# Optimization experiments

Hardware: AMD Instinct MI355X
Metric: run time of the kernel (lower is better)

The kernel has to match this reference:

```python
import jax, jax.numpy as jnp
import numpy as np

OUT, IN, BLK = 11008, 4096, 128

def setup_inputs() -> dict:
    key = jax.random.key(0)
    k1, k2, k3, k4, k5 = jax.random.split(key, 5)
    x = jax.random.normal(k1, (64, IN), dtype=jnp.float32)
    weight = jax.random.randint(k2, (OUT, IN // 2), 0, 256, dtype=jnp.int32)  # packed uint4 pairs
    scale = jax.random.uniform(k3, (OUT, 1, BLK), dtype=jnp.float32) * 0.01 + 1e-4
    zp = jax.random.randint(k4, (OUT, 1, BLK), 0, 16).astype(jnp.float32)
    bias = jax.random.normal(k5, (OUT,), dtype=jnp.float32)
    return {"x": x, "weight": weight, "scale": scale, "zp": zp, "bias": bias}

def reference(x, weight, scale, zp, bias):
    dtype = x.dtype
    # unpack: high nibble first, then low nibble (interleaved along in_features)
    w_h = (weight >> 4) & 15
    w_l = weight & 15
    w_unpacked = jnp.stack((w_h, w_l), axis=-1).reshape(OUT, IN)
    # block-wise dequant: scale/zp shaped [OUT, 1, BLK], broadcast over block index dim
    w_blocked = w_unpacked.reshape(OUT, IN // BLK, BLK).astype(dtype)
    w_rec = ((w_blocked - zp.astype(dtype)) * scale.astype(dtype)).reshape(OUT, IN)
    return x @ w_rec.T + bias
```

## Files before the change

### kernel.cpp

```cpp
#include <hip/hip_runtime.h>

#define OUT_F 11008
#define IN_F  4096
#define PKW   2048
#define BLKQ  128
#define MROWS 64

typedef __attribute__((ext_vector_type(8))) short          s16x8;
typedef __attribute__((ext_vector_type(8))) unsigned short u16x8;
typedef __attribute__((ext_vector_type(4))) float          f32x4;
typedef __attribute__((ext_vector_type(4))) int            i32x4;

__device__ __forceinline__ unsigned short f2bf(float f) {
    union { float f; unsigned u; } v; v.f = f;
    unsigned r = v.u + 0x8000u + ((v.u >> 16) & 1u);
    return (unsigned short)(r >> 16);
}

__global__ void prep_xfrag(const float* __restrict__ x, unsigned short* __restrict__ xf) {
    int kb   = blockIdx.x;
    int t    = threadIdx.x;
    int mt   = t >> 6;
    int lane = t & 63;
    int m  = mt * 16 + (lane & 15);
    int k0 = kb * 32 + (lane >> 4) * 8;
    const float* xp = x + m * IN_F + k0;
    f32x4 a = *(const f32x4*)(xp);
    f32x4 b = *(const f32x4*)(xp + 4);
    u16x8 v;
    v[0] = f2bf(a[0]); v[1] = f2bf(a[1]); v[2] = f2bf(a[2]); v[3] = f2bf(a[3]);
    v[4] = f2bf(b[0]); v[5] = f2bf(b[1]); v[6] = f2bf(b[2]); v[7] = f2bf(b[3]);
    *(u16x8*)(xf + (size_t)((kb * 4 + mt) * 64 + lane) * 8) = v;
}

__global__ __launch_bounds__(256) void qlin_main(
    const int*   __restrict__ wq,
    const float* __restrict__ scale,
    const float* __restrict__ zp,
    const float* __restrict__ bias,
    const unsigned short* __restrict__ xf,
    float* __restrict__ out)
{
    __shared__ __align__(16) unsigned short smem[4 * 16 * 136];

    const int t      = threadIdx.x;
    const int o_base = blockIdx.x * 16;
    const int wave   = t >> 6;
    const int lane   = t & 63;

    const int d      = t & 3;
    const int row_r  = (t >> 2) & 15;
    const int region = t >> 6;

    float s[32], zs[32];
    {
        const float* sp = scale + (size_t)(o_base + row_r) * BLKQ + d * 32;
        const float* zpp = zp   + (size_t)(o_base + row_r) * BLKQ + d * 32;
        #pragma unroll
        for (int i = 0; i < 8; ++i) {
            f32x4 sv = *(const f32x4*)(sp  + i * 4);
            f32x4 zv = *(const f32x4*)(zpp + i * 4);
            #pragma unroll
            for (int c = 0; c < 4; ++c) {
                s [i * 4 + c] = sv[c];
                zs[i * 4 + c] = zv[c] * sv[c];
            }
        }
    }

    const int* wbase = wq + (size_t)(o_base + row_r) * PKW + region * 512 + d * 16;
    unsigned short* myw = smem + (region * 16 + row_r) * 136 + d * 32;

    f32x4 acc[4];
    #pragma unroll
    for (int mt = 0; mt < 4; ++mt) acc[mt] = (f32x4){0.f, 0.f, 0.f, 0.f};

    i32x4 wreg[4];
    #pragma unroll
    for (int q = 0; q < 4; ++q) wreg[q] = *(const i32x4*)(wbase + q * 4);

    const s16x8* xfv = (const s16x8*)xf;
    const unsigned short* bbase = smem + (wave * 16 + (lane & 15)) * 136;
    const int quad = lane >> 4;

    for (int tt = 0; tt < 8; ++tt) {
        __syncthreads();

        #pragma unroll
        for (int q = 0; q < 4; ++q) {
            u16x8 ob;
            #pragma unroll
            for (int pp = 0; pp < 4; ++pp) {
                unsigned dw = (unsigned)wreg[q][pp];
                int p = q * 4 + pp;
                float fh = (float)((dw >> 4) & 15u);
                float fl = (float)(dw & 15u);
                ob[2 * pp]     = f2bf(fmaf(fh, s[2 * p],     -zs[2 * p]));
                ob[2 * pp + 1] = f2bf(fmaf(fl, s[2 * p + 1], -zs[2 * p + 1]));
            }
            *(u16x8*)(myw + q * 8) = ob;
        }

        if (tt < 7) {
            const int* nb = wbase + (tt + 1) * 64;
            #pragma unroll
            for (int q = 0; q < 4; ++q) wreg[q] = *(const i32x4*)(nb + q * 4);
        }

        __syncthreads();

        #pragma unroll
        for (int q0 = 0; q0 < 4; ++q0) {
            s16x8 bfrag = *(const s16x8*)(bbase + q0 * 32 + quad * 8);
            int kb = wave * 32 + tt * 4 + q0;
            #pragma unroll
            for (int mt = 0; mt < 4; ++mt) {
                s16x8 afrag = xfv[(size_t)(kb * 4 + mt) * 64 + lane];
                acc[mt] = __builtin_amdgcn_mfma_f32_16x16x32_bf16(afrag, bfrag, acc[mt], 0, 0, 0);
            }
        }
    }

    __syncthreads();
    float* lf = (float*)smem;
    {
        const int col = lane & 15;
        #pragma unroll
        for (int mt = 0; mt < 4; ++mt) {
            #pragma unroll
            for (int r = 0; r < 4; ++r) {
                int m = mt * 16 + quad * 4 + r;
                lf[wave * 1024 + m * 16 + col] = acc[mt][r];
            }
        }
    }
    __syncthreads();
    #pragma unroll
    for (int p = 0; p < 4; ++p) {
        int e = p * 256 + t;
        int m = e >> 4, col = e & 15;
        float v = lf[e] + lf[1024 + e] + lf[2048 + e] + lf[3072 + e] + bias[o_base + col];
        out[(size_t)m * OUT_F + o_base + col] = v;
    }
}

extern "C" void kernel_launch(void* const* d_in, const int* in_sizes, int n_in,
                              void* d_out, int out_size, void* d_ws, size_t ws_size,
                              hipStream_t stream) {
    const float* x     = (const float*)d_in[0];
    const int*   wq    = (const int*)d_in[1];
    const float* scale = (const float*)d_in[2];
    const float* zpv   = (const float*)d_in[3];
    const float* bias  = (const float*)d_in[4];
    float* out = (float*)d_out;
    unsigned short* xf = (unsigned short*)d_ws;

    prep_xfrag<<<128, 256, 0, stream>>>(x, xf);
    qlin_main<<<OUT_F / 16, 256, 0, stream>>>(wq, scale, zpv, bias, xf, out);
}
```

Before: 159.8 us.

## Dequantize weights directly into MFMA B fragments and double-buffer loads

Each lane now loads the packed weights and scale/zero-point values that match its own MFMA B-fragment position and dequantizes them in registers. This removes the LDS staging buffer and the two barriers per iteration. The activation fragments and the next weight group are prefetched into double-buffered registers so global loads overlap the MFMA work. The cost is more register pressure and smaller, strided weight loads per lane (16-byte reads at a 64-byte stride), which may coalesce less well than before.

```diff
diff --git a/kernel.cpp b/kernel.cpp
--- a/kernel.cpp
+++ b/kernel.cpp
@@ -4,7 +4,6 @@
 #define IN_F  4096
 #define PKW   2048
 #define BLKQ  128
-#define MROWS 64
 
 typedef __attribute__((ext_vector_type(8))) short          s16x8;
 typedef __attribute__((ext_vector_type(8))) unsigned short u16x8;
@@ -41,97 +40,89 @@
     const unsigned short* __restrict__ xf,
     float* __restrict__ out)
 {
-    __shared__ __align__(16) unsigned short smem[4 * 16 * 136];
+    __shared__ float lsum[4 * 1024];
 
     const int t      = threadIdx.x;
     const int o_base = blockIdx.x * 16;
     const int wave   = t >> 6;
     const int lane   = t & 63;
+    const int o_r    = lane & 15;
+    const int quad   = lane >> 4;
+    const int o      = o_base + o_r;
 
-    const int d      = t & 3;
-    const int row_r  = (t >> 2) & 15;
-    const int region = t >> 6;
-
-    float s[32], zs[32];
+    float s[4][8], zs[4][8];
     {
-        const float* sp = scale + (size_t)(o_base + row_r) * BLKQ + d * 32;
-        const float* zpp = zp   + (size_t)(o_base + row_r) * BLKQ + d * 32;
+        const float* sp  = scale + (size_t)o * BLKQ + quad * 8;
+        const float* zpp = zp    + (size_t)o * BLKQ + quad * 8;
         #pragma unroll
-        for (int i = 0; i < 8; ++i) {
-            f32x4 sv = *(const f32x4*)(sp  + i * 4);
-            f32x4 zv = *(const f32x4*)(zpp + i * 4);
+        for (int c4 = 0; c4 < 4; ++c4) {
+            f32x4 s0 = *(const f32x4*)(sp  + c4 * 32);
+            f32x4 s1 = *(const f32x4*)(sp  + c4 * 32 + 4);
+            f32x4 z0 = *(const f32x4*)(zpp + c4 * 32);
+            f32x4 z1 = *(const f32x4*)(zpp + c4 * 32 + 4);
             #pragma unroll
-            for (int c = 0; c < 4; ++c) {
-                s [i * 4 + c] = sv[c];
-                zs[i * 4 + c] = zv[c] * sv[c];
+            for (int i = 0; i < 4; ++i) {
+                s [c4][i]     = s0[i];  zs[c4][i]     = z0[i] * s0[i];
+                s [c4][i + 4] = s1[i];  zs[c4][i + 4] = z1[i] * s1[i];
             }
         }
     }
 
-    const int* wbase = wq + (size_t)(o_base + row_r) * PKW + region * 512 + d * 16;
-    unsigned short* myw = smem + (region * 16 + row_r) * 136 + d * 32;
+    const int* wb = wq + (size_t)o * PKW + wave * 512 + quad * 4;
+    const s16x8* xfv = (const s16x8*)xf;
+    const int kb0 = wave * 32;
 
     f32x4 acc[4];
     #pragma unroll
     for (int mt = 0; mt < 4; ++mt) acc[mt] = (f32x4){0.f, 0.f, 0.f, 0.f};
 
-    i32x4 wreg[4];
+    i32x4 wgrp[2][4];
+    s16x8 af[2][4];
+
     #pragma unroll
-    for (int q = 0; q < 4; ++q) wreg[q] = *(const i32x4*)(wbase + q * 4);
+    for (int cc = 0; cc < 4; ++cc) wgrp[0][cc] = *(const i32x4*)(wb + cc * 16);
+    #pragma unroll
+    for (int mt = 0; mt < 4; ++mt) af[0][mt] = xfv[(size_t)((kb0 * 4 + mt) * 64) + lane];
 
-    const s16x8* xfv = (const s16x8*)xf;
-    const unsigned short* bbase = smem + (wave * 16 + (lane & 15)) * 136;
-    const int quad = lane >> 4;
-
-    for (int tt = 0; tt < 8; ++tt) {
-        __syncthreads();
-
+    #pragma unroll
+    for (int g = 0; g < 8; ++g) {
+        const int pg = g & 1;
+        if (g < 7) {
+            const int* nb = wb + (g + 1) * 64;
+            #pragma unroll
+            for (int cc = 0; cc < 4; ++cc) wgrp[pg ^ 1][cc] = *(const i32x4*)(nb + cc * 16);
+        }
         #pragma unroll
-        for (int q = 0; q < 4; ++q) {
-            u16x8 ob;
+        for (int cc = 0; cc < 4; ++cc) {
+            const int kk = g * 4 + cc;
+            const int pb = kk & 1;
+            if (kk < 31) {
+                const int kbn = kb0 + kk + 1;
+                #pragma unroll
+                for (int mt = 0; mt < 4; ++mt)
+                    af[pb ^ 1][mt] = xfv[(size_t)((kbn * 4 + mt) * 64) + lane];
+            }
+            s16x8 bfr;
             #pragma unroll
-            for (int pp = 0; pp < 4; ++pp) {
-                unsigned dw = (unsigned)wreg[q][pp];
-                int p = q * 4 + pp;
+            for (int d = 0; d < 4; ++d) {
+                unsigned dw = (unsigned)wgrp[pg][cc][d];
                 float fh = (float)((dw >> 4) & 15u);
                 float fl = (float)(dw & 15u);
-                ob[2 * pp]     = f2bf(fmaf(fh, s[2 * p],     -zs[2 * p]));
-                ob[2 * pp + 1] = f2bf(fmaf(fl, s[2 * p + 1], -zs[2 * p + 1]));
+                bfr[2 * d]     = (short)f2bf(fmaf(fh, s[cc][2 * d],     -zs[cc][2 * d]));
+                bfr[2 * d + 1] = (short)f2bf(fmaf(fl, s[cc][2 * d + 1], -zs[cc][2 * d + 1]));
             }
-            *(u16x8*)(myw + q * 8) = ob;
-        }
-
-        if (tt < 7) {
-            const int* nb = wbase + (tt + 1) * 64;
             #pragma unroll
-            for (int q = 0; q < 4; ++q) wreg[q] = *(const i32x4*)(nb + q * 4);
-        }
-
-        __syncthreads();
-
-        #pragma unroll
-        for (int q0 = 0; q0 < 4; ++q0) {
-            s16x8 bfrag = *(const s16x8*)(bbase + q0 * 32 + quad * 8);
-            int kb = wave * 32 + tt * 4 + q0;
-            #pragma unroll
-            for (int mt = 0; mt < 4; ++mt) {
-                s16x8 afrag = xfv[(size_t)(kb * 4 + mt) * 64 + lane];
-                acc[mt] = __builtin_amdgcn_mfma_f32_16x16x32_bf16(afrag, bfrag, acc[mt], 0, 0, 0);
-            }
+            for (int mt = 0; mt < 4; ++mt)
+                acc[mt] = __builtin_amdgcn_mfma_f32_16x16x32_bf16(af[pb][mt], bfr, acc[mt], 0, 0, 0);
         }
     }
 
-    __syncthreads();
-    float* lf = (float*)smem;
-    {
-        const int col = lane & 15;
+    #pragma unroll
+    for (int mt = 0; mt < 4; ++mt) {
         #pragma unroll
-        for (int mt = 0; mt < 4; ++mt) {
-            #pragma unroll
-            for (int r = 0; r < 4; ++r) {
-                int m = mt * 16 + quad * 4 + r;
-                lf[wave * 1024 + m * 16 + col] = acc[mt][r];
-            }
+        for (int r = 0; r < 4; ++r) {
+            int m = mt * 16 + quad * 4 + r;
+            lsum[wave * 1024 + m * 16 + o_r] = acc[mt][r];
         }
     }
     __syncthreads();
@@ -139,7 +130,7 @@
     for (int p = 0; p < 4; ++p) {
         int e = p * 256 + t;
         int m = e >> 4, col = e & 15;
-        float v = lf[e] + lf[1024 + e] + lf[2048 + e] + lf[3072 + e] + bias[o_base + col];
+        float v = lsum[e] + lsum[1024 + e] + lsum[2048 + e] + lsum[3072 + e] + bias[o_base + col];
         out[(size_t)m * OUT_F + o_base + col] = v;
     }
 }
```

Measured after the change: 191.7 us. +19.9%, slower.

## Split K across blocks with 64-row tiles and separate combine kernel

Applied to the files above, without the earlier changes.

Each block now covers 64 output rows and one quarter of K, with waves splitting output rows instead of K so they share the same activation fragments. Partial sums go to a global workspace, and a new combine kernel sums the four partials and adds bias. This removes the in-block LDS reduction and redundant activation reads across waves, at the cost of extra global traffic for partials and an additional kernel launch.

```diff
diff --git a/kernel.cpp b/kernel.cpp
--- a/kernel.cpp
+++ b/kernel.cpp
@@ -4,7 +4,8 @@
 #define IN_F  4096
 #define PKW   2048
 #define BLKQ  128
-#define MROWS 64
+#define NTILE 172
+#define XFOFF (512 * 1024)
 
 typedef __attribute__((ext_vector_type(8))) short          s16x8;
 typedef __attribute__((ext_vector_type(8))) unsigned short u16x8;
@@ -37,25 +38,26 @@
     const int*   __restrict__ wq,
     const float* __restrict__ scale,
     const float* __restrict__ zp,
-    const float* __restrict__ bias,
     const unsigned short* __restrict__ xf,
-    float* __restrict__ out)
+    float* __restrict__ part)
 {
-    __shared__ __align__(16) unsigned short smem[4 * 16 * 136];
+    __shared__ __align__(16) unsigned short smem[64 * 136];
 
     const int t      = threadIdx.x;
-    const int o_base = blockIdx.x * 16;
+    const int tile   = blockIdx.x >> 2;
+    const int kq     = blockIdx.x & 3;
+    const int o_base = tile * 64;
     const int wave   = t >> 6;
     const int lane   = t & 63;
+    const int quad   = lane >> 4;
 
-    const int d      = t & 3;
-    const int row_r  = (t >> 2) & 15;
-    const int region = t >> 6;
+    const int d     = t & 3;
+    const int row_r = t >> 2;
 
     float s[32], zs[32];
     {
-        const float* sp = scale + (size_t)(o_base + row_r) * BLKQ + d * 32;
-        const float* zpp = zp   + (size_t)(o_base + row_r) * BLKQ + d * 32;
+        const float* sp  = scale + (size_t)(o_base + row_r) * BLKQ + d * 32;
+        const float* zpp = zp    + (size_t)(o_base + row_r) * BLKQ + d * 32;
         #pragma unroll
         for (int i = 0; i < 8; ++i) {
             f32x4 sv = *(const f32x4*)(sp  + i * 4);
@@ -68,8 +70,8 @@
         }
     }
 
-    const int* wbase = wq + (size_t)(o_base + row_r) * PKW + region * 512 + d * 16;
-    unsigned short* myw = smem + (region * 16 + row_r) * 136 + d * 32;
+    const int* wbase = wq + (size_t)(o_base + row_r) * PKW + kq * 512 + d * 16;
+    unsigned short* myw = smem + row_r * 136 + d * 32;
 
     f32x4 acc[4];
     #pragma unroll
@@ -81,7 +83,6 @@
 
     const s16x8* xfv = (const s16x8*)xf;
     const unsigned short* bbase = smem + (wave * 16 + (lane & 15)) * 136;
-    const int quad = lane >> 4;
 
     for (int tt = 0; tt < 8; ++tt) {
         __syncthreads();
@@ -112,7 +113,7 @@
         #pragma unroll
         for (int q0 = 0; q0 < 4; ++q0) {
             s16x8 bfrag = *(const s16x8*)(bbase + q0 * 32 + quad * 8);
-            int kb = wave * 32 + tt * 4 + q0;
+            int kb = kq * 32 + tt * 4 + q0;
             #pragma unroll
             for (int mt = 0; mt < 4; ++mt) {
                 s16x8 afrag = xfv[(size_t)(kb * 4 + mt) * 64 + lane];
@@ -121,27 +122,29 @@
         }
     }
 
-    __syncthreads();
-    float* lf = (float*)smem;
-    {
-        const int col = lane & 15;
+    const int oc = o_base + wave * 16 + (lane & 15);
+    float* pp = part + (size_t)kq * (64 * OUT_F) + oc;
+    #pragma unroll
+    for (int mt = 0; mt < 4; ++mt) {
         #pragma unroll
-        for (int mt = 0; mt < 4; ++mt) {
-            #pragma unroll
-            for (int r = 0; r < 4; ++r) {
-                int m = mt * 16 + quad * 4 + r;
-                lf[wave * 1024 + m * 16 + col] = acc[mt][r];
-            }
+        for (int r = 0; r < 4; ++r) {
+            pp[(size_t)(mt * 16 + quad * 4 + r) * OUT_F] = acc[mt][r];
         }
     }
-    __syncthreads();
-    #pragma unroll
-    for (int p = 0; p < 4; ++p) {
-        int e = p * 256 + t;
-        int m = e >> 4, col = e & 15;
-        float v = lf[e] + lf[1024 + e] + lf[2048 + e] + lf[3072 + e] + bias[o_base + col];
-        out[(size_t)m * OUT_F + o_base + col] = v;
-    }
+}
+
+__global__ __launch_bounds__(256) void combine(
+    const float* __restrict__ part, const float* __restrict__ bias,
+    float* __restrict__ out)
+{
+    int i = blockIdx.x * 256 + threadIdx.x;
+    const f32x4* p = (const f32x4*)part;
+    f32x4 v = p[i];
+    v += p[176128 + i];
+    v += p[2 * 176128 + i];
+    v += p[3 * 176128 + i];
+    f32x4 b = ((const f32x4*)bias)[i % 2752];
+    ((f32x4*)out)[i] = v + b;
 }
 
 extern "C" void kernel_launch(void* const* d_in, const int* in_sizes, int n_in,
@@ -154,7 +157,9 @@
     const float* bias  = (const float*)d_in[4];
     float* out = (float*)d_out;
     unsigned short* xf = (unsigned short*)d_ws;
+    float* part = (float*)((char*)d_ws + XFOFF);
 
     prep_xfrag<<<128, 256, 0, stream>>>(x, xf);
-    qlin_main<<<OUT_F / 16, 256, 0, stream>>>(wq, scale, zpv, bias, xf, out);
+    qlin_main<<<NTILE * 4, 256, 0, stream>>>(wq, scale, zpv, xf, part);
+    combine<<<688, 256, 0, stream>>>(part, bias, out);
 }
```

New measurement: 166.4 us. 4.1% more time.
